# Kernel optimization log

Hardware: AMD Instinct MI355X
Metric: run time of the kernel (lower is better)

The kernel has to match this reference:

```python
import jax, jax.numpy as jnp
import numpy as np

B, T, S = 32, 200, 256          # batch, decoder steps, encoder (memory) length
L = 512                          # latent_dims
U = 2 * L                        # LSTM units / attention units / attention_layer_size
E = 512                          # encoder memory feature dim
M = 80                           # mel_bins


def setup_inputs() -> dict:
    key = jax.random.key(0)
    ks = jax.random.split(key, 16)
    s = 0.05
    inputs = jax.random.normal(ks[0], (B, T, M), jnp.float32)
    memory = jax.random.normal(ks[1], (B, S, E), jnp.float32)
    # pre-net: Dense(2L, relu) -> Dropout -> Dense(L, relu) -> Dropout
    W1 = jax.random.normal(ks[2], (M, 2 * L), jnp.float32) * s
    b1 = jnp.zeros((2 * L,), jnp.float32)
    W2 = jax.random.normal(ks[3], (2 * L, L), jnp.float32) * s
    b2 = jnp.zeros((L,), jnp.float32)
    # LSTMCell(2L): input = concat(prenet_out [L], attention [U=2L]) -> 3L
    Wx = jax.random.normal(ks[4], (3 * L, 4 * U), jnp.float32) * s
    Wh = jax.random.normal(ks[5], (U, 4 * U), jnp.float32) * s
    b_lstm = jnp.zeros((4 * U,), jnp.float32)
    # Bahdanau attention (units=U): memory_layer, query_layer (no bias), score vector v
    Wm = jax.random.normal(ks[6], (E, U), jnp.float32) * s
    Wq = jax.random.normal(ks[7], (U, U), jnp.float32) * s
    v_att = jax.random.normal(ks[8], (U,), jnp.float32) * s
    # attention_layer (Dense, no bias): concat(cell_output [U], context [E]) -> U
    Wa = jax.random.normal(ks[9], (U + E, U), jnp.float32) * s
    # output projection to mel bins
    Wp = jax.random.normal(ks[10], (U, M), jnp.float32) * s
    bp = jnp.zeros((M,), jnp.float32)
    return dict(inputs=inputs, memory=memory, W1=W1, b1=b1, W2=W2, b2=b2,
                Wx=Wx, Wh=Wh, b_lstm=b_lstm, Wm=Wm, Wq=Wq, v_att=v_att,
                Wa=Wa, Wp=Wp, bp=bp)


def reference(inputs, memory, W1, b1, W2, b2, Wx, Wh, b_lstm, Wm, Wq, v_att, Wa, Wp, bp):
    # pre-net (inference: dropout is identity)
    x = jax.nn.relu(inputs @ W1 + b1)
    x = jax.nn.relu(x @ W2 + b2)                       # [B,T,L]
    keys = memory @ Wm                                 # precomputed attention keys [B,S,U]

    def step(carry, xt):
        h, c, attn = carry
        cell_in = jnp.concatenate([xt, attn], axis=-1)  # [B, 3L]
        z = cell_in @ Wx + h @ Wh + b_lstm              # [B, 4U]
        i, f, g, o = jnp.split(z, 4, axis=-1)
        c_new = jax.nn.sigmoid(f) * c + jax.nn.sigmoid(i) * jnp.tanh(g)
        h_new = jax.nn.sigmoid(o) * jnp.tanh(c_new)
        # Bahdanau additive attention
        q = h_new @ Wq                                  # [B,U]
        score = jnp.einsum('u,bsu->bs', v_att, jnp.tanh(keys + q[:, None, :]))
        align = jax.nn.softmax(score, axis=-1)          # [B,S]
        ctx = jnp.einsum('bs,bse->be', align, memory)   # [B,E]
        attn_new = jnp.concatenate([h_new, ctx], axis=-1) @ Wa  # [B,U]
        return (h_new, c_new, attn_new), attn_new

    init = (jnp.zeros((B, U), x.dtype), jnp.zeros((B, U), x.dtype), jnp.zeros((B, U), x.dtype))
    xs = jnp.swapaxes(x, 0, 1)                          # [T,B,L]
    (h, c, attn), ys = jax.lax.scan(step, init, xs)
    outs = jnp.swapaxes(ys, 0, 1)                       # [B,T,U]
    mel = outs @ Wp + bp                                # [B,T,M]
    return (mel, h, c, attn)
```

## Files before the change

### kernel.cpp

```cpp
#include <hip/hip_runtime.h>


typedef unsigned short us16;
typedef unsigned int u32;
typedef unsigned long long u64;
typedef __attribute__((ext_vector_type(8))) short bf16x8;
typedef __attribute__((ext_vector_type(4))) float f32x4;

#define MFMA16 __builtin_amdgcn_mfma_f32_16x16x32_bf16
#define AGT __HIP_MEMORY_SCOPE_AGENT

__device__ __forceinline__ us16 f2bf(float f){
  u32 u = __builtin_bit_cast(u32, f);
  u += 0x7fffu + ((u >> 16) & 1u);
  return (us16)(u >> 16);
}
__device__ __forceinline__ float bf2f(us16 h){
  return __builtin_bit_cast(float, ((u32)h) << 16);
}
__device__ __forceinline__ float h2f(us16 u){
  _Float16 h = __builtin_bit_cast(_Float16, u); return (float)h;
}
__device__ __forceinline__ us16 f2h(float f){
  _Float16 h = (_Float16)f; return __builtin_bit_cast(us16, h);
}
__device__ __forceinline__ void split3(float v, us16& s0, us16& s1, us16& s2){
  s0 = f2bf(v); float r = v - bf2f(s0);
  s1 = f2bf(r); r -= bf2f(s1);
  s2 = f2bf(r);
}
__device__ __forceinline__ float tanh_fast(float x){
  float e = __expf(-2.f * fmaxf(x, -40.f));
  return (1.f - e) / (1.f + e);
}

__device__ __forceinline__ u32 aload32(const u32* p){
  return __hip_atomic_load(p, __ATOMIC_RELAXED, AGT);
}
__device__ __forceinline__ void astoref(float* p, float v){
  __hip_atomic_store(p, v, __ATOMIC_RELAXED, AGT);
}
__device__ __forceinline__ void aaddf(float* p, float v){
  __hip_atomic_fetch_add(p, v, __ATOMIC_RELAXED, AGT);
}
__device__ __forceinline__ bf16x8 pin_reg(bf16x8 v){
  f32x4 t = __builtin_bit_cast(f32x4, v);
  asm volatile("" : "+v"(t));
  return __builtin_bit_cast(bf16x8, t);
}
__device__ __forceinline__ void f32_frag3(const float* p, float rs,
                                          bf16x8& f0, bf16x8& f1, bf16x8& f2){
  float4 t0 = *(const float4*)p;
  float4 t1 = *(const float4*)(p + 4);
  float tf[8] = {t0.x, t0.y, t0.z, t0.w, t1.x, t1.y, t1.z, t1.w};
#pragma unroll
  for (int i = 0; i < 8; ++i){
    float v = tf[i] * rs;
    us16 s0, s1, s2; split3(v, s0, s1, s2);
    f0[i] = (short)s0; f1[i] = (short)s1; f2[i] = (short)s2;
  }
}

#define OFF_WTA    0ull
#define OFF_WQT    50331648ull
#define OFF_X2P    56623104ull
#define OFF_KEYH   76283904ull
#define OFF_KEYL   93061120ull
#define OFF_X1     76283904ull
#define OFF_HIST   109838336ull
#define OFF_HROLL  129597440ull
#define OFF_UCROLL 155942912ull
#define OFF_SROLL  169115648ull
#define OFF_QROLL  169141376ull
#define OFF_CBUF   195355776ull
#define OFF_WAPN   195486848ull
#define OFF_BPERM  195732608ull
#define OFF_BAR    195748992ull
#define TOTAL_WS   195750016ull

#define WTPL 8388608ull
#define WQPL 1048576ull
#define X2PL 3276800ull

__global__ void k_zero_init(float* hroll0, float* ucroll, float* sroll,
                            float* cbuf, u32* bar){
  u32 id = blockIdx.x * 256u + threadIdx.x;
  const u32 gs = 65536u;
  for (u32 i = id; i < 32768u;   i += gs) hroll0[i] = 0.f;
  for (u32 i = id; i < 3293184u; i += gs) ucroll[i] = 0.f;
  for (u32 i = id; i < 6432u;    i += gs) sroll[i]  = (i < 32u) ? 1.f : 0.f;
  for (u32 i = id; i < 32768u;   i += gs) cbuf[i]   = 0.f;
  for (u32 i = id; i < 256u;     i += gs) bar[i]    = 0u;
}

__global__ void k_bperm(const float* __restrict__ bl, float* __restrict__ bpm){
  int c = blockIdx.x * 256 + threadIdx.x;
  if (c < 4096) bpm[((c & 1023) << 2) | (c >> 10)] = bl[c];
}

__global__ void k_transp3(const float* __restrict__ src, us16* __restrict__ dst,
                          int srows, int scols, int ldd, long long pstride, int perm){
  __shared__ float tile[32][33];
  int bx = blockIdx.x * 32, by = blockIdx.y * 32;
  int tx = threadIdx.x & 31, ty = threadIdx.x >> 5;
#pragma unroll
  for (int i = 0; i < 4; ++i){
    int r = by + ty + i * 8, c = bx + tx;
    tile[ty + i * 8][tx] = (r < srows && c < scols) ? src[(size_t)r * scols + c] : 0.f;
  }
  __syncthreads();
#pragma unroll
  for (int i = 0; i < 4; ++i){
    int c = bx + ty + i * 8;
    int r = by + tx;
    if (c < scols && r < srows){
      int oc = perm ? (((c & 1023) << 2) | (c >> 10)) : c;
      float v = tile[tx][ty + i * 8];
      us16 s0, s1, s2; split3(v, s0, s1, s2);
      size_t base = (size_t)oc * ldd + r;
      dst[base] = s0; dst[(size_t)pstride + base] = s1; dst[2ull * pstride + base] = s2;
    }
  }
}

template<int NP, int AF, int BF>
__global__ void __launch_bounds__(256)
k_gemm3(const void* __restrict__ Ap, const void* __restrict__ Bp, void* __restrict__ outp,
        int M, int N, int K, int mode, const float* __restrict__ aux, int ldd){
  __shared__ us16 At[NP][128][72];
  __shared__ us16 Bt[NP][64][72];
  const int tid = threadIdx.x, wv = tid >> 6, lane = tid & 63;
  const int r0 = lane & 15, kg = lane >> 4;
  const int rb = blockIdx.x * 128, cb = blockIdx.y * 64;
  f32x4 acc[2][4];
#pragma unroll
  for (int a = 0; a < 2; ++a)
#pragma unroll
    for (int b = 0; b < 4; ++b) acc[a][b] = (f32x4){0.f, 0.f, 0.f, 0.f};

  const int nkt = (K + 63) >> 6;
  for (int kt = 0; kt < nkt; ++kt){
    const int kb = kt * 64;
    for (int e = tid; e < 8192; e += 256){
      int r = e >> 6, k = e & 63, ga = rb + r, gk = kb + k;
      bool ok = (ga < M) && (gk < K);
      if constexpr (AF){
        float v = ok ? ((const float*)Ap)[(size_t)ga * K + gk] : 0.f;
        us16 s0, s1, s2; split3(v, s0, s1, s2);
        At[0][r][k] = s0;
        if constexpr (NP == 3){ At[1][r][k] = s1; At[2][r][k] = s2; }
      } else {
        At[0][r][k] = ok ? ((const us16*)Ap)[(size_t)ga * K + gk] : (us16)0;
      }
    }
    for (int e = tid; e < 4096; e += 256){
      int kr = e >> 6, c = e & 63, gk = kb + kr, gc = cb + c;
      bool ok = (gk < K) && (gc < N);
      if constexpr (BF){
        float v = ok ? ((const float*)Bp)[(size_t)gk * N + gc] : 0.f;
        us16 s0, s1, s2; split3(v, s0, s1, s2);
        Bt[0][c][kr] = s0;
        if constexpr (NP == 3){ Bt[1][c][kr] = s1; Bt[2][c][kr] = s2; }
      } else {
        Bt[0][c][kr] = ok ? ((const us16*)Bp)[(size_t)gk * N + gc] : (us16)0;
      }
    }
    __syncthreads();
#pragma unroll
    for (int kk = 0; kk < 64; kk += 32){
      bf16x8 af[NP][2];
#pragma unroll
      for (int p = 0; p < NP; ++p){
        af[p][0] = *(const bf16x8*)&At[p][wv * 32 + r0][kk + kg * 8];
        af[p][1] = *(const bf16x8*)&At[p][wv * 32 + 16 + r0][kk + kg * 8];
      }
#pragma unroll
      for (int cf = 0; cf < 4; ++cf){
        bf16x8 bv[NP];
#pragma unroll
        for (int p = 0; p < NP; ++p) bv[p] = *(const bf16x8*)&Bt[p][cf * 16 + r0][kk + kg * 8];
#pragma unroll
        for (int rf = 0; rf < 2; ++rf){
          acc[rf][cf] = MFMA16(af[0][rf], bv[0], acc[rf][cf], 0, 0, 0);
          if constexpr (NP == 3){
            acc[rf][cf] = MFMA16(af[0][rf], bv[1], acc[rf][cf], 0, 0, 0);
            acc[rf][cf] = MFMA16(af[1][rf], bv[0], acc[rf][cf], 0, 0, 0);
            acc[rf][cf] = MFMA16(af[0][rf], bv[2], acc[rf][cf], 0, 0, 0);
            acc[rf][cf] = MFMA16(af[1][rf], bv[1], acc[rf][cf], 0, 0, 0);
            acc[rf][cf] = MFMA16(af[2][rf], bv[0], acc[rf][cf], 0, 0, 0);
          }
        }
      }
    }
    __syncthreads();
  }
  us16* o16 = (us16*)outp; float* of = (float*)outp;
#pragma unroll
  for (int rf = 0; rf < 2; ++rf)
#pragma unroll
    for (int cf = 0; cf < 4; ++cf)
#pragma unroll
      for (int i = 0; i < 4; ++i){
        int r = rb + wv * 32 + rf * 16 + kg * 4 + i;
        int c = cb + cf * 16 + r0;
        if (r >= M || c >= N) continue;
        float v = acc[rf][cf][i];
        if (mode == 0){
          of[(size_t)r * ldd + c] = fmaxf(v + aux[c], 0.f);
        } else if (mode == 1){
          v = fmaxf(v + aux[c], 0.f);
          us16 s0, s1, s2; split3(v, s0, s1, s2);
          size_t b2 = (size_t)r * ldd + c;
          o16[b2] = s0; o16[X2PL + b2] = s1; o16[2 * X2PL + b2] = s2;
        } else if (mode == 2){
          us16 hh = f2h(v); float rem = v - h2f(hh); us16 hl = f2h(rem);
          size_t b2 = (size_t)r * 1024 + c;
          o16[b2] = hh; o16[WTPL + b2] = hl;
        } else if (mode == 3){
          float w = v + (r < 1024 ? aux[(size_t)r * 4096 + c] : 0.f);
          int pc = (c & 1023) * 4 + (c >> 10);
          us16 s0, s1, s2; split3(w, s0, s1, s2);
          size_t b2 = (size_t)pc * 2048 + 512 + r;
          o16[b2] = s0; o16[WTPL + b2] = s1; o16[2 * WTPL + b2] = s2;
        } else if (mode == 4){
          o16[(size_t)r * ldd + c] = f2bf(v);
        } else if (mode == 5){
          of[((size_t)(r & 31) * 200 + (r >> 5)) * 80 + c] = v + aux[c];
        } else {
          of[(size_t)r * ldd + c] = v;
        }
      }
}

__device__ __forceinline__ void gbar(u32* bar, u32 ep, int tid, int blk){
  __syncthreads();
  if (tid == 0){
    asm volatile("s_waitcnt vmcnt(0)" ::: "memory");
    u32 g = (u32)(blk >> 5);
    u32 old = __hip_atomic_fetch_add(&bar[g * 32], 1u, __ATOMIC_RELAXED, AGT);
    if (old == 32u * ep - 1u){
      u32 r = __hip_atomic_fetch_add(&bar[248], 1u, __ATOMIC_RELAXED, AGT);
      if (r == 8u * ep - 1u)
        __hip_atomic_store(&bar[252], ep, __ATOMIC_RELAXED, AGT);
    }
    while (aload32(&bar[252]) < ep) __builtin_amdgcn_s_sleep(1);
    __builtin_amdgcn_sched_barrier(0);
  }
  __syncthreads();
}

struct CoopA {
  const us16 *wta, *wqt, *x2p, *kh, *kl;
  const float *mem, *vatt, *bperm;
  us16 *hist;
  float *hroll, *ucroll, *sroll, *qroll, *cbuf;
  u32 *bar;
};

__global__ void __launch_bounds__(512, 2) k_coop(CoopA a){
  __shared__ us16 khi[32][1024];
  __shared__ us16 klo[32][1024];
  __shared__ float zp[8][512];
  __shared__ float esc[32];
  __shared__ float rs_lds[32];

  __builtin_amdgcn_fence(__ATOMIC_ACQUIRE, "agent");

  const int tid = threadIdx.x, blk = blockIdx.x;
  const int wv = tid >> 6, lane = tid & 63;
  const int r0 = lane & 15, kg = lane >> 4;
  const int cb_b = blk >> 3, cb_s0 = (blk & 7) * 32;
  const int colbase = blk * 16;
  const int u0 = lane * 16;

  bf16x8 wr[8][3];
#pragma unroll
  for (int ks = 0; ks < 8; ++ks){
    const size_t wb = (size_t)(colbase + r0) * 2048 + (size_t)wv * 256 + ks * 32 + kg * 8;
#pragma unroll
    for (int p = 0; p < 3; ++p)
      wr[ks][p] = pin_reg(*(const bf16x8*)&a.wta[(size_t)p * WTPL + wb]);
  }
  bf16x8 wq[4][3];
  if (blk < 64){
#pragma unroll
    for (int ks = 0; ks < 4; ++ks){
      const size_t wb = (size_t)(colbase + r0) * 1024 + (size_t)wv * 128 + ks * 32 + kg * 8;
#pragma unroll
      for (int p = 0; p < 3; ++p)
        wq[ks][p] = pin_reg(*(const bf16x8*)&a.wqt[(size_t)p * WQPL + wb]);
    }
  }

  {
    const size_t kbase = ((size_t)(cb_b * 256 + cb_s0)) * 1024;
    for (int i = tid; i < 4096; i += 512){
      int r = i >> 7, c8 = (i & 127) * 8;
      *(bf16x8*)&khi[r][c8] = *(const bf16x8*)&a.kh[kbase + (size_t)r * 1024 + c8];
      *(bf16x8*)&klo[r][c8] = *(const bf16x8*)&a.kl[kbase + (size_t)r * 1024 + c8];
    }
  }
  __syncthreads();

  u32 ep = 0;
  for (int t = 0; t < 200; ++t){
    {
      if (tid < 32) rs_lds[tid] = 1.f / a.sroll[(size_t)t * 32 + tid];
      __syncthreads();
      if (tid < 64){
        int flat = blk * 64 + tid;
        int b = flat >> 9, e = flat & 511;
        float v = a.ucroll[(size_t)t * 16384 + flat];
        a.hist[(size_t)(t * 32 + b) * 1536 + 1024 + e] = f2bf(v * rs_lds[b]);
      }
      f32x4 acc0 = (f32x4){0.f,0.f,0.f,0.f}, acc1 = acc0;
#pragma unroll
      for (int ks = 0; ks < 8; ++ks){
        const int k0 = wv * 256 + ks * 32;
        const int kf = k0 + kg * 8;
        bf16x8 w0 = wr[ks][0], w1 = wr[ks][1], w2 = wr[ks][2];
        bf16x8 a00, a01, a02, a10, a11, a12;
        if (wv < 2){
          const size_t xb0 = ((size_t)r0 * 200 + t) * 512 + kf;
          const size_t xb1 = ((size_t)(r0 + 16) * 200 + t) * 512 + kf;
          a00 = *(const bf16x8*)&a.x2p[xb0];
          a01 = *(const bf16x8*)&a.x2p[X2PL + xb0];
          a02 = *(const bf16x8*)&a.x2p[2 * X2PL + xb0];
          a10 = *(const bf16x8*)&a.x2p[xb1];
          a11 = *(const bf16x8*)&a.x2p[X2PL + xb1];
          a12 = *(const bf16x8*)&a.x2p[2 * X2PL + xb1];
        } else if (wv < 6){
          const int hk = kf - 512;
          const float* hp0 = a.hroll + (size_t)t * 32768 + (size_t)r0 * 1024 + hk;
          f32_frag3(hp0,         1.f, a00, a01, a02);
          f32_frag3(hp0 + 16384, 1.f, a10, a11, a12);
        } else {
          const int ek = kf - 1536;
          const float* up = a.ucroll + (size_t)t * 16384 + (size_t)r0 * 512 + ek;
          f32_frag3(up,        rs_lds[r0],      a00, a01, a02);
          f32_frag3(up + 8192, rs_lds[r0 + 16], a10, a11, a12);
        }
        acc0 = MFMA16(a00, w0, acc0, 0,0,0); acc0 = MFMA16(a00, w1, acc0, 0,0,0);
        acc0 = MFMA16(a01, w0, acc0, 0,0,0); acc0 = MFMA16(a00, w2, acc0, 0,0,0);
        acc0 = MFMA16(a01, w1, acc0, 0,0,0); acc0 = MFMA16(a02, w0, acc0, 0,0,0);
        acc1 = MFMA16(a10, w0, acc1, 0,0,0); acc1 = MFMA16(a10, w1, acc1, 0,0,0);
        acc1 = MFMA16(a11, w0, acc1, 0,0,0); acc1 = MFMA16(a10, w2, acc1, 0,0,0);
        acc1 = MFMA16(a11, w1, acc1, 0,0,0); acc1 = MFMA16(a12, w0, acc1, 0,0,0);
      }
#pragma unroll
      for (int i = 0; i < 4; ++i){
        zp[wv][(kg * 4 + i) * 16 + r0]      = acc0[i];
        zp[wv][(16 + kg * 4 + i) * 16 + r0] = acc1[i];
      }
      __syncthreads();
      float z = 0.f;
#pragma unroll
      for (int w = 0; w < 8; ++w) z += zp[w][tid];
      z += a.bperm[colbase + (tid & 15)];
      __syncthreads();
      zp[0][tid] = z;
      __syncthreads();
      if (tid < 128){
        int b = tid >> 2, ul = tid & 3, u = blk * 4 + ul;
        float zi = zp[0][b * 16 + ul * 4 + 0];
        float zf = zp[0][b * 16 + ul * 4 + 1];
        float zg = zp[0][b * 16 + ul * 4 + 2];
        float zo = zp[0][b * 16 + ul * 4 + 3];
        float co = a.cbuf[b * 1024 + u];
        float cn = (1.f / (1.f + expf(-zf))) * co + (1.f / (1.f + expf(-zi))) * tanhf(zg);
        float hn = (1.f / (1.f + expf(-zo))) * tanhf(cn);
        a.cbuf[b * 1024 + u] = cn;
        astoref(&a.hroll[(size_t)(t + 1) * 32768 + b * 1024 + u], hn);
        us16 s0, s1, s2; split3(hn, s0, s1, s2);
        a.hist[((size_t)(t + 1) * 32 + b) * 1536 + u] = s0;
      }
    }
    gbar(a.bar, ++ep, tid, blk);

    if (blk < 64){
      f32x4 acc0 = (f32x4){0.f,0.f,0.f,0.f}, acc1 = acc0;
#pragma unroll
      for (int ks = 0; ks < 4; ++ks){
        const int kf = wv * 128 + ks * 32 + kg * 8;
        bf16x8 w0 = wq[ks][0], w1 = wq[ks][1], w2 = wq[ks][2];
        bf16x8 a00, a01, a02, a10, a11, a12;
        const float* hp0 = a.hroll + (size_t)(t + 1) * 32768 + (size_t)r0 * 1024 + kf;
        f32_frag3(hp0,         1.f, a00, a01, a02);
        f32_frag3(hp0 + 16384, 1.f, a10, a11, a12);
        acc0 = MFMA16(a00, w0, acc0, 0,0,0); acc0 = MFMA16(a00, w1, acc0, 0,0,0);
        acc0 = MFMA16(a01, w0, acc0, 0,0,0); acc0 = MFMA16(a00, w2, acc0, 0,0,0);
        acc0 = MFMA16(a01, w1, acc0, 0,0,0); acc0 = MFMA16(a02, w0, acc0, 0,0,0);
        acc1 = MFMA16(a10, w0, acc1, 0,0,0); acc1 = MFMA16(a10, w1, acc1, 0,0,0);
        acc1 = MFMA16(a11, w0, acc1, 0,0,0); acc1 = MFMA16(a10, w2, acc1, 0,0,0);
        acc1 = MFMA16(a11, w1, acc1, 0,0,0); acc1 = MFMA16(a12, w0, acc1, 0,0,0);
      }
#pragma unroll
      for (int i = 0; i < 4; ++i){
        zp[wv][(kg * 4 + i) * 16 + r0]      = acc0[i];
        zp[wv][(16 + kg * 4 + i) * 16 + r0] = acc1[i];
      }
      __syncthreads();
      float q = 0.f;
#pragma unroll
      for (int w = 0; w < 8; ++w) q += zp[w][tid];
      astoref(&a.qroll[(size_t)t * 32768 + (size_t)(tid >> 4) * 1024 + colbase + (tid & 15)], q);
    }
    gbar(a.bar, ++ep, tid, blk);

    {
      float qv[16], vv[16];
      {
        const float* qp = a.qroll + (size_t)t * 32768 + (size_t)cb_b * 1024 + u0;
        float4 q0 = *(const float4*)qp;
        float4 q1 = *(const float4*)(qp + 4);
        float4 q2 = *(const float4*)(qp + 8);
        float4 q3 = *(const float4*)(qp + 12);
        qv[0]=q0.x; qv[1]=q0.y; qv[2]=q0.z; qv[3]=q0.w;
        qv[4]=q1.x; qv[5]=q1.y; qv[6]=q1.z; qv[7]=q1.w;
        qv[8]=q2.x; qv[9]=q2.y; qv[10]=q2.z; qv[11]=q2.w;
        qv[12]=q3.x; qv[13]=q3.y; qv[14]=q3.z; qv[15]=q3.w;
        float4 v0 = *(const float4*)(a.vatt + u0);
        float4 v1 = *(const float4*)(a.vatt + u0 + 4);
        float4 v2 = *(const float4*)(a.vatt + u0 + 8);
        float4 v3 = *(const float4*)(a.vatt + u0 + 12);
        vv[0]=v0.x; vv[1]=v0.y; vv[2]=v0.z; vv[3]=v0.w;
        vv[4]=v1.x; vv[5]=v1.y; vv[6]=v1.z; vv[7]=v1.w;
        vv[8]=v2.x; vv[9]=v2.y; vv[10]=v2.z; vv[11]=v2.w;
        vv[12]=v3.x; vv[13]=v3.y; vv[14]=v3.z; vv[15]=v3.w;
      }
#pragma unroll
      for (int m = 0; m < 4; ++m){
        const int sl = wv * 4 + m;
        bf16x8 h0 = *(const bf16x8*)&khi[sl][u0];
        bf16x8 h1 = *(const bf16x8*)&khi[sl][u0 + 8];
        bf16x8 l0 = *(const bf16x8*)&klo[sl][u0];
        bf16x8 l1 = *(const bf16x8*)&klo[sl][u0 + 8];
        float part = 0.f;
#pragma unroll
        for (int j = 0; j < 8; ++j){
          float kva = h2f((us16)h0[j]) + h2f((us16)l0[j]);
          part += vv[j] * tanh_fast(kva + qv[j]);
          float kvb = h2f((us16)h1[j]) + h2f((us16)l1[j]);
          part += vv[8 + j] * tanh_fast(kvb + qv[8 + j]);
        }
#pragma unroll
        for (int off = 32; off; off >>= 1) part += __shfl_xor(part, off);
        if (lane == 0) esc[sl] = __expf(part);
      }
      __syncthreads();
      if (tid == 0){
        float bs = 0.f;
#pragma unroll
        for (int i = 0; i < 32; ++i) bs += esc[i];
        aaddf(&a.sroll[(size_t)(t + 1) * 32 + cb_b], bs);
      }
      {
        float ac0 = 0.f, ac1 = 0.f, ac2 = 0.f, ac3 = 0.f;
        const float* mrow = a.mem + ((size_t)(cb_b * 256 + cb_s0)) * 512 + tid;
#pragma unroll
        for (int j = 0; j < 32; j += 4){
          ac0 += esc[j]     * mrow[(size_t)j * 512];
          ac1 += esc[j + 1] * mrow[(size_t)(j + 1) * 512];
          ac2 += esc[j + 2] * mrow[(size_t)(j + 2) * 512];
          ac3 += esc[j + 3] * mrow[(size_t)(j + 3) * 512];
        }
        aaddf(&a.ucroll[(size_t)(t + 1) * 16384 + cb_b * 512 + tid], (ac0 + ac1) + (ac2 + ac3));
      }
    }
    gbar(a.bar, ++ep, tid, blk);
  }

  {
    if (tid < 32) rs_lds[tid] = 1.f / a.sroll[(size_t)200 * 32 + tid];
    __syncthreads();
    if (tid < 64){
      int flat = blk * 64 + tid;
      int b = flat >> 9, e = flat & 511;
      float v = a.ucroll[(size_t)200 * 16384 + flat];
      a.hist[(size_t)(200 * 32 + b) * 1536 + 1024 + e] = f2bf(v * rs_lds[b]);
    }
  }
}

__global__ void k_copy_hc(const float* __restrict__ h, const float* __restrict__ c,
                          float* __restrict__ out){
  int i = blockIdx.x * 256 + threadIdx.x;
  if (i < 32768){
    out[512000 + i] = h[i];
    out[544768 + i] = c[i];
  }
}

extern "C" void kernel_launch(void* const* d_in, const int* in_sizes, int n_in,
                              void* d_out, int out_size, void* d_ws, size_t ws_size,
                              hipStream_t stream){
  const float* inputs = (const float*)d_in[0];
  const float* memory = (const float*)d_in[1];
  const float* W1     = (const float*)d_in[2];
  const float* b1     = (const float*)d_in[3];
  const float* W2     = (const float*)d_in[4];
  const float* b2     = (const float*)d_in[5];
  const float* Wx     = (const float*)d_in[6];
  const float* Wh     = (const float*)d_in[7];
  const float* b_lstm = (const float*)d_in[8];
  const float* Wm     = (const float*)d_in[9];
  const float* Wq     = (const float*)d_in[10];
  const float* v_att  = (const float*)d_in[11];
  const float* Wa     = (const float*)d_in[12];
  const float* Wp     = (const float*)d_in[13];
  const float* bp     = (const float*)d_in[14];
  float* out = (float*)d_out;
  char* ws = (char*)d_ws;
  if (ws_size < TOTAL_WS) return;

  us16* WTA    = (us16*)(ws + OFF_WTA);
  us16* WQT    = (us16*)(ws + OFF_WQT);
  us16* X2P    = (us16*)(ws + OFF_X2P);
  us16* KEYH   = (us16*)(ws + OFF_KEYH);
  float* X1    = (float*)(ws + OFF_X1);
  us16* HIST   = (us16*)(ws + OFF_HIST);
  float* HROLL = (float*)(ws + OFF_HROLL);
  float* UCROLL= (float*)(ws + OFF_UCROLL);
  float* SROLL = (float*)(ws + OFF_SROLL);
  float* QROLL = (float*)(ws + OFF_QROLL);
  float* CBUF  = (float*)(ws + OFF_CBUF);
  us16* WAPN   = (us16*)(ws + OFF_WAPN);
  float* BPM   = (float*)(ws + OFF_BPERM);
  u32*  BAR    = (u32*)(ws + OFF_BAR);

  k_zero_init<<<256, 256, 0, stream>>>(HROLL, UCROLL, SROLL, CBUF, BAR);
  k_bperm<<<16, 256, 0, stream>>>(b_lstm, BPM);
  k_transp3<<<dim3(32, 32), 256, 0, stream>>>(Wq, WQT, 1024, 1024, 1024, (long long)WQPL, 0);
  k_transp3<<<dim3(128, 16), 256, 0, stream>>>(Wx, WTA, 512, 4096, 2048, (long long)WTPL, 1);

  k_gemm3<3,1,1><<<dim3(12, 64), 256, 0, stream>>>(Wa, Wx + (size_t)512 * 4096, WTA,
                                                   1536, 4096, 1024, 3, Wh, 0);
  k_gemm3<3,1,1><<<dim3(12, 2), 256, 0, stream>>>(Wa, Wp, WAPN, 1536, 80, 1024, 4, nullptr, 80);
  k_gemm3<3,1,1><<<dim3(50, 16), 256, 0, stream>>>(inputs, W1, X1, 6400, 1024, 80, 0, b1, 1024);
  k_gemm3<3,1,1><<<dim3(50, 8), 256, 0, stream>>>(X1, W2, X2P, 6400, 512, 1024, 1, b2, 512);
  k_gemm3<3,1,1><<<dim3(64, 16), 256, 0, stream>>>(memory, Wm, KEYH, 8192, 1024, 512, 2, nullptr, 1024);

  CoopA ca;
  ca.wta = WTA; ca.wqt = WQT; ca.x2p = X2P; ca.kh = KEYH; ca.kl = KEYH + WTPL;
  ca.mem = memory; ca.vatt = v_att; ca.bperm = BPM;
  ca.hist = HIST; ca.hroll = HROLL; ca.ucroll = UCROLL; ca.sroll = SROLL;
  ca.qroll = QROLL; ca.cbuf = CBUF; ca.bar = BAR;
  void* args[] = {(void*)&ca};
  hipLaunchCooperativeKernel((const void*)k_coop, dim3(256), dim3(512), args, 0, stream);

  k_gemm3<1,0,0><<<dim3(50, 2), 256, 0, stream>>>(HIST + (size_t)32 * 1536, WAPN, out,
                                                  6400, 80, 1536, 5, bp, 0);
  k_gemm3<1,0,1><<<dim3(1, 16), 256, 0, stream>>>(HIST + (size_t)200 * 32 * 1536, Wa,
                                                  out + 577536, 32, 1024, 1536, 6, nullptr, 1024);
  k_copy_hc<<<128, 256, 0, stream>>>(HROLL + (size_t)200 * 32768, CBUF, out);
}
```

Measured before the change: 12.45 ms.

## Replace global barriers with per-block flags and pre-split h into bf16 planes

Replaces the hierarchical atomic grid barrier with per-block epoch flags. Only the 64 q-producing blocks wait on the h flags, and every block waits only on the q or context flags it needs. The new hidden state is stored already split into three bf16 planes, so consumers load fragments directly instead of re-splitting fp32 values. The Wq weights are reloaded from memory each step instead of being pinned in registers, and launch bounds drop to one block per SM. This trades register pressure and barrier latency for extra global loads and many spinning pollers.

```diff
diff --git a/kernel.cpp b/kernel.cpp
--- a/kernel.cpp
+++ b/kernel.cpp
@@ -37,11 +37,29 @@
 __device__ __forceinline__ u32 aload32(const u32* p){
   return __hip_atomic_load(p, __ATOMIC_RELAXED, AGT);
 }
+__device__ __forceinline__ u64 aload64(const u64* p){
+  return __hip_atomic_load(p, __ATOMIC_RELAXED, AGT);
+}
+__device__ __forceinline__ void astore16(us16* p, us16 v){
+  __hip_atomic_store(p, v, __ATOMIC_RELAXED, AGT);
+}
 __device__ __forceinline__ void astoref(float* p, float v){
   __hip_atomic_store(p, v, __ATOMIC_RELAXED, AGT);
 }
+__device__ __forceinline__ void sigflag(u32* p, u32 v){
+  __hip_atomic_store(p, v, __ATOMIC_RELAXED, AGT);
+}
 __device__ __forceinline__ void aaddf(float* p, float v){
   __hip_atomic_fetch_add(p, v, __ATOMIC_RELAXED, AGT);
+}
+__device__ __forceinline__ bf16x8 ld16(const us16* p){
+  return *(const bf16x8*)p;
+}
+__device__ __forceinline__ float4 aloadf4(const float* p){
+  union { u64 u[2]; float4 f; } t;
+  const u64* q = (const u64*)p;
+  t.u[0] = aload64(q); t.u[1] = aload64(q + 1);
+  return t.f;
 }
 __device__ __forceinline__ bf16x8 pin_reg(bf16x8 v){
   f32x4 t = __builtin_bit_cast(f32x4, v);
@@ -68,29 +86,29 @@
 #define OFF_KEYL   93061120ull
 #define OFF_X1     76283904ull
 #define OFF_HIST   109838336ull
-#define OFF_HROLL  129597440ull
-#define OFF_UCROLL 155942912ull
-#define OFF_SROLL  169115648ull
-#define OFF_QROLL  169141376ull
-#define OFF_CBUF   195355776ull
-#define OFF_WAPN   195486848ull
-#define OFF_BPERM  195732608ull
-#define OFF_BAR    195748992ull
-#define TOTAL_WS   195750016ull
+#define OFF_HPR    129597440ull
+#define OFF_UCR    169115648ull
+#define OFF_SR     182288384ull
+#define OFF_QB     182314112ull
+#define OFF_CB     182445184ull
+#define OFF_HF     182576256ull
+#define OFF_WAPN   182707328ull
+#define OFF_BPERM  182953088ull
+#define OFF_FLG    182969472ull
+#define TOTAL_WS   183018624ull
 
 #define WTPL 8388608ull
 #define WQPL 1048576ull
 #define X2PL 3276800ull
 
-__global__ void k_zero_init(float* hroll0, float* ucroll, float* sroll,
-                            float* cbuf, u32* bar){
+__global__ void k_zero_init(u32* hpr0, float* ucr, float* sr, float* cbuf, u32* flg){
   u32 id = blockIdx.x * 256u + threadIdx.x;
   const u32 gs = 65536u;
-  for (u32 i = id; i < 32768u;   i += gs) hroll0[i] = 0.f;
-  for (u32 i = id; i < 3293184u; i += gs) ucroll[i] = 0.f;
-  for (u32 i = id; i < 6432u;    i += gs) sroll[i]  = (i < 32u) ? 1.f : 0.f;
-  for (u32 i = id; i < 32768u;   i += gs) cbuf[i]   = 0.f;
-  for (u32 i = id; i < 256u;     i += gs) bar[i]    = 0u;
+  for (u32 i = id; i < 49152u;   i += gs) hpr0[i] = 0u;
+  for (u32 i = id; i < 3293184u; i += gs) ucr[i]  = 0.f;
+  for (u32 i = id; i < 6432u;    i += gs) sr[i]   = (i < 32u) ? 1.f : 0.f;
+  for (u32 i = id; i < 32768u;   i += gs) cbuf[i] = 0.f;
+  for (u32 i = id; i < 12288u;   i += gs) flg[i]  = 0u;
 }
 
 __global__ void k_bperm(const float* __restrict__ bl, float* __restrict__ bpm){
@@ -232,32 +250,17 @@
       }
 }
 
-__device__ __forceinline__ void gbar(u32* bar, u32 ep, int tid, int blk){
-  __syncthreads();
-  if (tid == 0){
-    asm volatile("s_waitcnt vmcnt(0)" ::: "memory");
-    u32 g = (u32)(blk >> 5);
-    u32 old = __hip_atomic_fetch_add(&bar[g * 32], 1u, __ATOMIC_RELAXED, AGT);
-    if (old == 32u * ep - 1u){
-      u32 r = __hip_atomic_fetch_add(&bar[248], 1u, __ATOMIC_RELAXED, AGT);
-      if (r == 8u * ep - 1u)
-        __hip_atomic_store(&bar[252], ep, __ATOMIC_RELAXED, AGT);
-    }
-    while (aload32(&bar[252]) < ep) __builtin_amdgcn_s_sleep(1);
-    __builtin_amdgcn_sched_barrier(0);
-  }
-  __syncthreads();
-}
-
 struct CoopA {
   const us16 *wta, *wqt, *x2p, *kh, *kl;
   const float *mem, *vatt, *bperm;
-  us16 *hist;
-  float *hroll, *ucroll, *sroll, *qroll, *cbuf;
-  u32 *bar;
+  us16 *hist, *hpr;
+  float *ucr, *sr, *qb, *cbuf, *hf32;
+  u32 *flg;
 };
 
-__global__ void __launch_bounds__(512, 2) k_coop(CoopA a){
+#define DRAIN asm volatile("s_waitcnt vmcnt(0)" ::: "memory")
+
+__global__ void __launch_bounds__(512, 1) k_coop(CoopA a){
   __shared__ us16 khi[32][1024];
   __shared__ us16 klo[32][1024];
   __shared__ float zp[8][512];
@@ -272,6 +275,9 @@
   const int cb_b = blk >> 3, cb_s0 = (blk & 7) * 32;
   const int colbase = blk * 16;
   const int u0 = lane * 16;
+  u32* hfl = a.flg;
+  u32* qfl = a.flg + 4096;
+  u32* cfl = a.flg + 8192;
 
   bf16x8 wr[8][3];
 #pragma unroll
@@ -280,16 +286,6 @@
 #pragma unroll
     for (int p = 0; p < 3; ++p)
       wr[ks][p] = pin_reg(*(const bf16x8*)&a.wta[(size_t)p * WTPL + wb]);
-  }
-  bf16x8 wq[4][3];
-  if (blk < 64){
-#pragma unroll
-    for (int ks = 0; ks < 4; ++ks){
-      const size_t wb = (size_t)(colbase + r0) * 1024 + (size_t)wv * 128 + ks * 32 + kg * 8;
-#pragma unroll
-      for (int p = 0; p < 3; ++p)
-        wq[ks][p] = pin_reg(*(const bf16x8*)&a.wqt[(size_t)p * WQPL + wb]);
-    }
   }
 
   {
@@ -302,15 +298,15 @@
   }
   __syncthreads();
 
-  u32 ep = 0;
   for (int t = 0; t < 200; ++t){
+    const u32 ep = (u32)(t + 1);
     {
-      if (tid < 32) rs_lds[tid] = 1.f / a.sroll[(size_t)t * 32 + tid];
+      if (tid < 32) rs_lds[tid] = 1.f / a.sr[(size_t)t * 32 + tid];
       __syncthreads();
       if (tid < 64){
         int flat = blk * 64 + tid;
         int b = flat >> 9, e = flat & 511;
-        float v = a.ucroll[(size_t)t * 16384 + flat];
+        float v = a.ucr[(size_t)t * 16384 + flat];
         a.hist[(size_t)(t * 32 + b) * 1536 + 1024 + e] = f2bf(v * rs_lds[b]);
       }
       f32x4 acc0 = (f32x4){0.f,0.f,0.f,0.f}, acc1 = acc0;
@@ -331,12 +327,16 @@
           a12 = *(const bf16x8*)&a.x2p[2 * X2PL + xb1];
         } else if (wv < 6){
           const int hk = kf - 512;
-          const float* hp0 = a.hroll + (size_t)t * 32768 + (size_t)r0 * 1024 + hk;
-          f32_frag3(hp0,         1.f, a00, a01, a02);
-          f32_frag3(hp0 + 16384, 1.f, a10, a11, a12);
+          const us16* hb = a.hpr + (size_t)t * 98304;
+          a00 = ld16(&hb[(size_t)r0 * 1024 + hk]);
+          a01 = ld16(&hb[32768 + (size_t)r0 * 1024 + hk]);
+          a02 = ld16(&hb[65536 + (size_t)r0 * 1024 + hk]);
+          a10 = ld16(&hb[(size_t)(r0 + 16) * 1024 + hk]);
+          a11 = ld16(&hb[32768 + (size_t)(r0 + 16) * 1024 + hk]);
+          a12 = ld16(&hb[65536 + (size_t)(r0 + 16) * 1024 + hk]);
         } else {
           const int ek = kf - 1536;
-          const float* up = a.ucroll + (size_t)t * 16384 + (size_t)r0 * 512 + ek;
+          const float* up = a.ucr + (size_t)t * 16384 + (size_t)r0 * 512 + ek;
           f32_frag3(up,        rs_lds[r0],      a00, a01, a02);
           f32_frag3(up + 8192, rs_lds[r0 + 16], a10, a11, a12);
         }
@@ -370,23 +370,37 @@
         float cn = (1.f / (1.f + expf(-zf))) * co + (1.f / (1.f + expf(-zi))) * tanhf(zg);
         float hn = (1.f / (1.f + expf(-zo))) * tanhf(cn);
         a.cbuf[b * 1024 + u] = cn;
-        astoref(&a.hroll[(size_t)(t + 1) * 32768 + b * 1024 + u], hn);
+        a.hf32[b * 1024 + u] = hn;
         us16 s0, s1, s2; split3(hn, s0, s1, s2);
         a.hist[((size_t)(t + 1) * 32 + b) * 1536 + u] = s0;
-      }
-    }
-    gbar(a.bar, ++ep, tid, blk);
+        us16* hb = a.hpr + (size_t)(t + 1) * 98304;
+        astore16(&hb[b * 1024 + u], s0);
+        astore16(&hb[32768 + b * 1024 + u], s1);
+        astore16(&hb[65536 + b * 1024 + u], s2);
+      }
+    }
+    DRAIN;
+    __syncthreads();
+    if (tid == 0) sigflag(&hfl[blk * 16], ep);
 
     if (blk < 64){
+      if (tid < 256) while (aload32(&hfl[tid * 16]) < ep) __builtin_amdgcn_s_sleep(1);
+      __syncthreads();
       f32x4 acc0 = (f32x4){0.f,0.f,0.f,0.f}, acc1 = acc0;
 #pragma unroll
       for (int ks = 0; ks < 4; ++ks){
         const int kf = wv * 128 + ks * 32 + kg * 8;
-        bf16x8 w0 = wq[ks][0], w1 = wq[ks][1], w2 = wq[ks][2];
-        bf16x8 a00, a01, a02, a10, a11, a12;
-        const float* hp0 = a.hroll + (size_t)(t + 1) * 32768 + (size_t)r0 * 1024 + kf;
-        f32_frag3(hp0,         1.f, a00, a01, a02);
-        f32_frag3(hp0 + 16384, 1.f, a10, a11, a12);
+        const size_t wb = (size_t)(colbase + r0) * 1024 + kf;
+        bf16x8 w0 = *(const bf16x8*)&a.wqt[wb];
+        bf16x8 w1 = *(const bf16x8*)&a.wqt[WQPL + wb];
+        bf16x8 w2 = *(const bf16x8*)&a.wqt[2 * WQPL + wb];
+        const us16* hb = a.hpr + (size_t)(t + 1) * 98304;
+        bf16x8 a00 = ld16(&hb[(size_t)r0 * 1024 + kf]);
+        bf16x8 a01 = ld16(&hb[32768 + (size_t)r0 * 1024 + kf]);
+        bf16x8 a02 = ld16(&hb[65536 + (size_t)r0 * 1024 + kf]);
+        bf16x8 a10 = ld16(&hb[(size_t)(r0 + 16) * 1024 + kf]);
+        bf16x8 a11 = ld16(&hb[32768 + (size_t)(r0 + 16) * 1024 + kf]);
+        bf16x8 a12 = ld16(&hb[65536 + (size_t)(r0 + 16) * 1024 + kf]);
         acc0 = MFMA16(a00, w0, acc0, 0,0,0); acc0 = MFMA16(a00, w1, acc0, 0,0,0);
         acc0 = MFMA16(a01, w0, acc0, 0,0,0); acc0 = MFMA16(a00, w2, acc0, 0,0,0);
         acc0 = MFMA16(a01, w1, acc0, 0,0,0); acc0 = MFMA16(a02, w0, acc0, 0,0,0);
@@ -403,18 +417,20 @@
       float q = 0.f;
 #pragma unroll
       for (int w = 0; w < 8; ++w) q += zp[w][tid];
-      astoref(&a.qroll[(size_t)t * 32768 + (size_t)(tid >> 4) * 1024 + colbase + (tid & 15)], q);
-    }
-    gbar(a.bar, ++ep, tid, blk);
+      astoref(&a.qb[(size_t)(tid >> 4) * 1024 + colbase + (tid & 15)], q);
+      DRAIN;
+      __syncthreads();
+      if (tid == 0) sigflag(&qfl[blk * 16], ep);
+    }
+    if (tid < 64) while (aload32(&qfl[tid * 16]) < ep) __builtin_amdgcn_s_sleep(1);
+    __syncthreads();
 
     {
       float qv[16], vv[16];
       {
-        const float* qp = a.qroll + (size_t)t * 32768 + (size_t)cb_b * 1024 + u0;
-        float4 q0 = *(const float4*)qp;
-        float4 q1 = *(const float4*)(qp + 4);
-        float4 q2 = *(const float4*)(qp + 8);
-        float4 q3 = *(const float4*)(qp + 12);
+        const float* qp = a.qb + (size_t)cb_b * 1024 + u0;
+        float4 q0 = aloadf4(qp), q1 = aloadf4(qp + 4);
+        float4 q2 = aloadf4(qp + 8), q3 = aloadf4(qp + 12);
         qv[0]=q0.x; qv[1]=q0.y; qv[2]=q0.z; qv[3]=q0.w;
         qv[4]=q1.x; qv[5]=q1.y; qv[6]=q1.z; qv[7]=q1.w;
         qv[8]=q2.x; qv[9]=q2.y; qv[10]=q2.z; qv[11]=q2.w;
@@ -452,7 +468,7 @@
         float bs = 0.f;
 #pragma unroll
         for (int i = 0; i < 32; ++i) bs += esc[i];
-        aaddf(&a.sroll[(size_t)(t + 1) * 32 + cb_b], bs);
+        aaddf(&a.sr[(size_t)(t + 1) * 32 + cb_b], bs);
       }
       {
         float ac0 = 0.f, ac1 = 0.f, ac2 = 0.f, ac3 = 0.f;
@@ -464,19 +480,23 @@
           ac2 += esc[j + 2] * mrow[(size_t)(j + 2) * 512];
           ac3 += esc[j + 3] * mrow[(size_t)(j + 3) * 512];
         }
-        aaddf(&a.ucroll[(size_t)(t + 1) * 16384 + cb_b * 512 + tid], (ac0 + ac1) + (ac2 + ac3));
-      }
-    }
-    gbar(a.bar, ++ep, tid, blk);
+        aaddf(&a.ucr[(size_t)(t + 1) * 16384 + cb_b * 512 + tid], (ac0 + ac1) + (ac2 + ac3));
+      }
+    }
+    DRAIN;
+    __syncthreads();
+    if (tid == 0) sigflag(&cfl[blk * 16], ep);
+    if (tid < 256) while (aload32(&cfl[tid * 16]) < ep) __builtin_amdgcn_s_sleep(1);
+    __syncthreads();
   }
 
   {
-    if (tid < 32) rs_lds[tid] = 1.f / a.sroll[(size_t)200 * 32 + tid];
+    if (tid < 32) rs_lds[tid] = 1.f / a.sr[(size_t)200 * 32 + tid];
     __syncthreads();
     if (tid < 64){
       int flat = blk * 64 + tid;
       int b = flat >> 9, e = flat & 511;
-      float v = a.ucroll[(size_t)200 * 16384 + flat];
+      float v = a.ucr[(size_t)200 * 16384 + flat];
       a.hist[(size_t)(200 * 32 + b) * 1536 + 1024 + e] = f2bf(v * rs_lds[b]);
     }
   }
@@ -519,16 +539,17 @@
   us16* KEYH   = (us16*)(ws + OFF_KEYH);
   float* X1    = (float*)(ws + OFF_X1);
   us16* HIST   = (us16*)(ws + OFF_HIST);
-  float* HROLL = (float*)(ws + OFF_HROLL);
-  float* UCROLL= (float*)(ws + OFF_UCROLL);
-  float* SROLL = (float*)(ws + OFF_SROLL);
-  float* QROLL = (float*)(ws + OFF_QROLL);
-  float* CBUF  = (float*)(ws + OFF_CBUF);
+  us16* HPR    = (us16*)(ws + OFF_HPR);
+  float* UCR   = (float*)(ws + OFF_UCR);
+  float* SR    = (float*)(ws + OFF_SR);
+  float* QB    = (float*)(ws + OFF_QB);
+  float* CB    = (float*)(ws + OFF_CB);
+  float* HF    = (float*)(ws + OFF_HF);
   us16* WAPN   = (us16*)(ws + OFF_WAPN);
   float* BPM   = (float*)(ws + OFF_BPERM);
-  u32*  BAR    = (u32*)(ws + OFF_BAR);
-
-  k_zero_init<<<256, 256, 0, stream>>>(HROLL, UCROLL, SROLL, CBUF, BAR);
+  u32*  FLG    = (u32*)(ws + OFF_FLG);
+
+  k_zero_init<<<256, 256, 0, stream>>>((u32*)HPR, UCR, SR, CB, FLG);
   k_bperm<<<16, 256, 0, stream>>>(b_lstm, BPM);
   k_transp3<<<dim3(32, 32), 256, 0, stream>>>(Wq, WQT, 1024, 1024, 1024, (long long)WQPL, 0);
   k_transp3<<<dim3(128, 16), 256, 0, stream>>>(Wx, WTA, 512, 4096, 2048, (long long)WTPL, 1);
@@ -543,8 +564,8 @@
   CoopA ca;
   ca.wta = WTA; ca.wqt = WQT; ca.x2p = X2P; ca.kh = KEYH; ca.kl = KEYH + WTPL;
   ca.mem = memory; ca.vatt = v_att; ca.bperm = BPM;
-  ca.hist = HIST; ca.hroll = HROLL; ca.ucroll = UCROLL; ca.sroll = SROLL;
-  ca.qroll = QROLL; ca.cbuf = CBUF; ca.bar = BAR;
+  ca.hist = HIST; ca.hpr = HPR; ca.ucr = UCR; ca.sr = SR;
+  ca.qb = QB; ca.cbuf = CB; ca.hf32 = HF; ca.flg = FLG;
   void* args[] = {(void*)&ca};
   hipLaunchCooperativeKernel((const void*)k_coop, dim3(256), dim3(512), args, 0, stream);
 
@@ -552,5 +573,5 @@
                                                   6400, 80, 1536, 5, bp, 0);
   k_gemm3<1,0,1><<<dim3(1, 16), 256, 0, stream>>>(HIST + (size_t)200 * 32 * 1536, Wa,
                                                   out + 577536, 32, 1024, 1536, 6, nullptr, 1024);
-  k_copy_hc<<<128, 256, 0, stream>>>(HROLL + (size_t)200 * 32768, CBUF, out);
-}
+  k_copy_hc<<<128, 256, 0, stream>>>(HF, CB, out);
+}
```

Measured after the change: 12.98 ms. 1.04x slower.
